# Kernel optimization log

Measured on AMD Instinct MI355X. Metric: run time of the kernel, lower is better.

Reference implementation:

```python
import jax, jax.numpy as jnp
import numpy as np

B, N, F_IN = 32, 1024, 64   # batch, num_nodes, diffusion_size[0]
K = 3                        # expansion_step
H = 2                        # num_heads
HID, RAW, OUT, CLS = 128, 128, 128, 2
D1, D2 = 128, 128            # diffusion_size[1], diffusion_size[2]
CAT = D1 + RAW               # concat dim fed to attention (h || h_prime) = 256


def setup_inputs() -> dict:
    key = jax.random.key(0)
    ks = jax.random.split(key, 40)
    g = lambda i, shape: jax.random.normal(ks[i], shape, dtype=jnp.float32) * 0.05
    inp = {
        'X': jax.random.normal(ks[0], (B, N, F_IN), dtype=jnp.float32),
        'A': jax.random.uniform(ks[1], (B, N, N), dtype=jnp.float32),
        # transition tensors / mixing weights (only the 2 layers used in forward)
        'T': g(2, (2, K, N, N)),
        'theta': jnp.full((2, K), 1.0 / K, dtype=jnp.float32),
        # raw feature projection
        'W_raw': g(3, (F_IN, RAW)), 'b_raw': jnp.zeros((RAW,), jnp.float32),
        # diffusion layer linears
        'Wd0': g(4, (F_IN, D1)), 'bd0': jnp.zeros((D1,), jnp.float32),
        'Wd1': g(5, (D1, D2)),   'bd1': jnp.zeros((D2,), jnp.float32),
        # final classifier
        'W_fin': g(6, (OUT, CLS)), 'b_fin': jnp.zeros((CLS,), jnp.float32),
    }
    # two CatMultiAttn blocks: q/k/v projections (CAT->HID), out proj (HID->OUT)
    i = 7
    for l in range(2):
        for nm in ('q', 'k', 'v'):
            inp[f'W{nm}{l}'] = g(i, (CAT, HID)); i += 1
            inp[f'b{nm}{l}'] = jnp.zeros((HID,), jnp.float32)
        inp[f'Wo{l}'] = g(i, (HID, OUT)); i += 1
        inp[f'bo{l}'] = jnp.zeros((OUT,), jnp.float32)
    return inp


def _diffusion(theta_l, T_l, h, A, W, b):
    # Q = sum_k theta_k * T_k  (generalized graph diffusion transition)
    Q = jnp.einsum('k,kij->ij', theta_l, T_l)          # [N,N]
    S = Q[None, :, :] * A                               # [B,N,N] mask by adjacency
    z = jnp.einsum('bij,bjf->bif', S, h)                # diffuse features
    return jax.nn.relu(z @ W + b)


def _cat_attn(h, hp, Wq, bq, Wk, bk, Wv, bv, Wo, bo):
    # concatenate diffused + embedding features, multi-head self-attn over nodes
    x = jnp.concatenate([h, hp], axis=-1)               # [B,N,CAT]
    b, n, _ = x.shape
    q = (x @ Wq + bq).reshape(b, n, H, HID // H)
    k = (x @ Wk + bk).reshape(b, n, H, HID // H)
    v = (x @ Wv + bv).reshape(b, n, H, HID // H)
    scale = jnp.asarray(1.0 / np.sqrt(HID // H), x.dtype)
    s = jnp.einsum('bnhd,bmhd->bhnm', q, k) * scale     # [B,H,N,N]
    p = jax.nn.softmax(s, axis=-1)
    ctx = jnp.einsum('bhnm,bmhd->bnhd', p, v).reshape(b, n, HID)
    return jax.nn.relu(ctx @ Wo + bo)


def reference(X, A, T, theta, W_raw, b_raw, Wd0, bd0, Wd1, bd1,
              W_fin, b_fin,
              Wq0, bq0, Wk0, bk0, Wv0, bv0, Wo0, bo0,
              Wq1, bq1, Wk1, bk1, Wv1, bv1, Wo1, bo1):
    theta_soft = jax.nn.softmax(theta, axis=-1)         # [2,K]
    h_prime = X @ W_raw + b_raw                          # [B,N,RAW]
    # layer 0
    h = _diffusion(theta_soft[0], T[0], X, A, Wd0, bd0)  # [B,N,D1]
    h_prime = _cat_attn(h, h_prime, Wq0, bq0, Wk0, bk0, Wv0, bv0, Wo0, bo0)
    # layer 1 (residual fusion)
    h = _diffusion(theta_soft[1], T[1], h, A, Wd1, bd1)  # [B,N,D2]
    h_prime = h_prime + _cat_attn(h, h_prime, Wq1, bq1, Wk1, bk1, Wv1, bv1, Wo1, bo1)
    return h_prime @ W_fin + b_fin                       # [B,N,CLS]
```

## Files before the change

### kernel.cpp

```cpp
#include <hip/hip_runtime.h>
#include <hip/hip_bf16.h>

typedef __hip_bfloat16 bf16;
typedef __attribute__((ext_vector_type(8))) short s8b;
typedef __attribute__((ext_vector_type(4))) short s4b;
typedef __attribute__((ext_vector_type(4))) float f4;

#define BB   32
#define NN   1024
#define FIN  64
#define HEADS 2
#define DH   64
#define HIDD 128
#define SZQ  ((size_t)BB * NN * HIDD)

__device__ __forceinline__ ushort f2bf(float x) {
    bf16 h = __float2bfloat16(x);
    return *(ushort*)&h;
}
__device__ __forceinline__ float bfbits2f(ushort h) {
    union { uint u; float f; } c; c.u = (uint)h << 16; return c.f;
}
__device__ __forceinline__ uint pk_bf16(float lo, float hi) {
    return (uint)f2bf(lo) | ((uint)f2bf(hi) << 16);
}
union U8 { short s[8]; s8b v; };
union U4 { short s[4]; s4b v; };
union UQ { ushort u[8]; s8b v; };

__global__ __launch_bounds__(256) void setup_kernel(
        const float* __restrict__ raw, const float* __restrict__ d0,
        const float* __restrict__ d1,
        const float* __restrict__ q0w, const float* __restrict__ k0w,
        const float* __restrict__ v0w, const float* __restrict__ o0w,
        const float* __restrict__ q1w, const float* __restrict__ k1w,
        const float* __restrict__ v1w, const float* __restrict__ o1w,
        ushort* __restrict__ Whi, ushort* __restrict__ Wlo,
        const float* __restrict__ T, const float* __restrict__ theta,
        ushort* __restrict__ Q0hi, ushort* __restrict__ Q0lo,
        ushort* __restrict__ Q1hi, ushort* __restrict__ Q1lo,
        const float* __restrict__ X,
        ushort* __restrict__ XT_hi, ushort* __restrict__ XT_lo) {
    __shared__ float tile[64][65];
    const int bid = blockIdx.x;
    const int t = threadIdx.x;
    if (bid < 1024) {
        int id = bid * 256 + t;
        const float* src; int K, off;
        if      (id <   8192) { src = raw; K =  64; off = 0; }
        else if (id <  16384) { src = d0;  K =  64; off = 8192; }
        else if (id <  32768) { src = d1;  K = 128; off = 16384; }
        else if (id <  65536) { src = q0w; K = 256; off = 32768; }
        else if (id <  98304) { src = k0w; K = 256; off = 65536; }
        else if (id < 131072) { src = v0w; K = 256; off = 98304; }
        else if (id < 147456) { src = o0w; K = 128; off = 131072; }
        else if (id < 180224) { src = q1w; K = 256; off = 147456; }
        else if (id < 212992) { src = k1w; K = 256; off = 180224; }
        else if (id < 245760) { src = v1w; K = 256; off = 212992; }
        else                  { src = o1w; K = 128; off = 245760; }
        int il = id - off;
        int k = il >> 7, c = il & 127;
        float w = src[il];
        ushort h = f2bf(w);
        Whi[off + c * K + k] = h;
        Wlo[off + c * K + k] = f2bf(w - bfbits2f(h));
    } else if (bid < 1536) {
        const int tb = bid - 1024;
        const int b  = tb >> 4;
        const int n0 = (tb & 15) * 64;
        {
            int nl = t >> 2, f0 = (t & 3) * 16;
            const float* xp = X + ((size_t)b * NN + n0 + nl) * 64 + f0;
#pragma unroll
            for (int i = 0; i < 16; i += 4)
                *(float4*)&tile[nl][f0 + i] = *(const float4*)(xp + i);
        }
        __syncthreads();
        {
            int f = t >> 2, n1 = (t & 3) * 16;
            U8 h0, h1, l0, l1;
#pragma unroll
            for (int i = 0; i < 16; i++) {
                float v = tile[n1 + i][f];
                ushort hh = f2bf(v);
                ushort ll = f2bf(v - bfbits2f(hh));
                if (i < 8) { h0.s[i] = (short)hh; l0.s[i] = (short)ll; }
                else       { h1.s[i - 8] = (short)hh; l1.s[i - 8] = (short)ll; }
            }
            size_t gb = ((size_t)b * 64 + f) * NN + n0 + n1;
            *(s8b*)&XT_hi[gb]     = h0.v;  *(s8b*)&XT_hi[gb + 8] = h1.v;
            *(s8b*)&XT_lo[gb]     = l0.v;  *(s8b*)&XT_lo[gb + 8] = l1.v;
        }
    } else {
        const int layer = (bid < 2048) ? 0 : 1;
        ushort* Qhi = layer ? Q1hi : Q0hi;
        ushort* Qlo = layer ? Q1lo : Q0lo;
        float t0 = theta[layer * 3 + 0];
        float t1 = theta[layer * 3 + 1];
        float t2 = theta[layer * 3 + 2];
        float m  = fmaxf(t0, fmaxf(t1, t2));
        float e0 = expf(t0 - m), e1 = expf(t1 - m), e2 = expf(t2 - m);
        float inv = 1.0f / (e0 + e1 + e2);
        e0 *= inv; e1 *= inv; e2 *= inv;
        size_t base = ((size_t)((bid - 1536) & 511) * 256 + t) * 8;
        const float* Tl = T + (size_t)layer * 3 * NN * NN;
        U8 hi, lo;
#pragma unroll
        for (int i = 0; i < 8; i++) {
            float q = e0 * Tl[base + i]
                    + e1 * Tl[base + i + (size_t)NN * NN]
                    + e2 * Tl[base + i + (size_t)2 * NN * NN];
            ushort hh = f2bf(q);
            hi.s[i] = (short)hh;
            lo.s[i] = (short)f2bf(q - bfbits2f(hh));
        }
        *(s8b*)&Qhi[base] = hi.v;
        *(s8b*)&Qlo[base] = lo.v;
    }
}

template<int F>
__global__ __launch_bounds__(512, 4) void diffusion_mfma_kernel(
        const ushort* __restrict__ Qhi, const ushort* __restrict__ Qlo,
        const float* __restrict__ A,
        const ushort* __restrict__ hT_hi, const ushort* __restrict__ hT_lo,
        float* __restrict__ z) {
    constexpr int SS  = 72;
    constexpr int NT  = F / 16;
    constexpr int TPW = NT / 2;
    __shared__ short Shi[64][SS], Slo[64][SS];
    __shared__ short Hhi[F][SS],  Hlo[F][SS];

    const int b  = blockIdx.x >> 4;
    const int i0 = (blockIdx.x & 15) * 64;
    const int t  = threadIdx.x;
    const int w  = t >> 6, lane = t & 63;
    const int quad = lane >> 4, c = lane & 15;
    const int mt = w >> 1, nh = w & 1;

    const int srow = t >> 3, scol = (t & 7) * 8;
    const float*  Ap = A   + ((size_t)b * NN + i0 + srow) * NN + scol;
    const ushort* Qh = Qhi + (size_t)(i0 + srow) * NN + scol;
    const ushort* Ql = Qlo + (size_t)(i0 + srow) * NN + scol;
    constexpr int HTR = 512 / F;
    constexpr int HJ  = 64 / HTR;
    constexpr int HV  = HJ / 8;
    const int hrow = t / HTR, hcol = (t % HTR) * HJ;
    const ushort* Hh = hT_hi + ((size_t)b * F + hrow) * NN + hcol;
    const ushort* Hl = hT_lo + ((size_t)b * F + hrow) * NN + hcol;

    f4 acc[TPW];
#pragma unroll
    for (int i = 0; i < TPW; i++) acc[i] = (f4){0.f, 0.f, 0.f, 0.f};

    float4 a0 = *(const float4*)Ap, a1 = *(const float4*)(Ap + 4);
    s8b hhv[HV], hlv[HV];
#pragma unroll
    for (int vv = 0; vv < HV; vv++) {
        hhv[vv] = *(const s8b*)(Hh + 8 * vv);
        hlv[vv] = *(const s8b*)(Hl + 8 * vv);
    }

#pragma unroll 1
    for (int j0 = 0; j0 < NN; j0 += 64) {
        UQ qh, ql;
        qh.v = *(const s8b*)(Qh + j0);
        ql.v = *(const s8b*)(Ql + j0);
        __syncthreads();
        {
            float av[8] = {a0.x, a0.y, a0.z, a0.w, a1.x, a1.y, a1.z, a1.w};
            U8 hi, lo;
#pragma unroll
            for (int i = 0; i < 8; i++) {
                float q = bfbits2f(qh.u[i]) + bfbits2f(ql.u[i]);
                float s = q * av[i];
                ushort hb = f2bf(s);
                hi.s[i] = (short)hb;
                lo.s[i] = (short)f2bf(s - bfbits2f(hb));
            }
            *(s8b*)&Shi[srow][scol] = hi.v;
            *(s8b*)&Slo[srow][scol] = lo.v;
#pragma unroll
            for (int vv = 0; vv < HV; vv++) {
                *(s8b*)&Hhi[hrow][hcol + 8 * vv] = hhv[vv];
                *(s8b*)&Hlo[hrow][hcol + 8 * vv] = hlv[vv];
            }
        }
        if (j0 + 64 < NN) {
            a0 = *(const float4*)(Ap + j0 + 64);
            a1 = *(const float4*)(Ap + j0 + 68);
#pragma unroll
            for (int vv = 0; vv < HV; vv++) {
                hhv[vv] = *(const s8b*)(Hh + j0 + 64 + 8 * vv);
                hlv[vv] = *(const s8b*)(Hl + j0 + 64 + 8 * vv);
            }
        }
        __syncthreads();

#pragma unroll
        for (int ks = 0; ks < 2; ks++) {
            s8b ahi = *(const s8b*)&Shi[mt * 16 + c][ks * 32 + quad * 8];
            s8b alo = *(const s8b*)&Slo[mt * 16 + c][ks * 32 + quad * 8];
#pragma unroll
            for (int tt = 0; tt < TPW; tt++) {
                const int nt = nh * TPW + tt;
                s8b bhi = *(const s8b*)&Hhi[nt * 16 + c][ks * 32 + quad * 8];
                s8b blo = *(const s8b*)&Hlo[nt * 16 + c][ks * 32 + quad * 8];
                acc[tt] = __builtin_amdgcn_mfma_f32_16x16x32_bf16(ahi, bhi, acc[tt], 0, 0, 0);
                acc[tt] = __builtin_amdgcn_mfma_f32_16x16x32_bf16(alo, bhi, acc[tt], 0, 0, 0);
                acc[tt] = __builtin_amdgcn_mfma_f32_16x16x32_bf16(ahi, blo, acc[tt], 0, 0, 0);
            }
        }
    }
#pragma unroll
    for (int tt = 0; tt < TPW; tt++)
#pragma unroll
        for (int r = 0; r < 4; r++)
            z[((size_t)b * NN + i0 + mt * 16 + quad * 4 + r) * F + (nh * TPW + tt) * 16 + c] = acc[tt][r];
}

template<int K1, int K2, int CB, bool RELU, bool RESID, int OMODE>
__global__ __launch_bounds__(256) void dense_mfma_kernel(
        const float* __restrict__ in1, const float* __restrict__ in2,
        const ushort* __restrict__ WT_hi, const ushort* __restrict__ WT_lo,
        const float* __restrict__ bias, const float* __restrict__ biask,
        const float* __restrict__ biasv,
        float* __restrict__ out, ushort* __restrict__ outq,
        ushort* __restrict__ hiT, ushort* __restrict__ loT,
        const float* __restrict__ Wfin, const float* __restrict__ bfin,
        float* __restrict__ fout) {
    constexpr int KD  = K1 + K2;
    constexpr int NKT = KD / 32;
    constexpr int NCT = CB / 16;
    __shared__ short Xhi[64][40], Xlo[64][40];
    __shared__ short Whi[CB][40], Wlo[CB][40];

    const int r0 = blockIdx.x * 64;
    const int c0 = blockIdx.y * CB;
    const int t  = threadIdx.x;
    const int w  = t >> 6, lane = t & 63;
    const int quad = lane >> 4, c = lane & 15;

    f4 acc[NCT];
#pragma unroll
    for (int i = 0; i < NCT; i++) acc[i] = (f4){0.f, 0.f, 0.f, 0.f};

    for (int kt = 0; kt < NKT; kt++) {
        const int k0 = kt * 32;
        __syncthreads();
        {
            int row = t >> 2, kk = (t & 3) * 8;
            int g = r0 + row;
            const float* p;
            if (K2 > 0) {
                int k = k0 + kk;
                p = (k < K1) ? (in1 + (size_t)g * K1 + k)
                             : (in2 + (size_t)g * K2 + (k - K1));
            } else {
                p = in1 + (size_t)g * K1 + k0 + kk;
            }
            float4 a = *(const float4*)p, bq = *(const float4*)(p + 4);
            float sv[8] = {a.x, a.y, a.z, a.w, bq.x, bq.y, bq.z, bq.w};
            U8 hi, lo;
#pragma unroll
            for (int i = 0; i < 8; i++) {
                ushort hh = f2bf(sv[i]);
                hi.s[i] = (short)hh;
                lo.s[i] = (short)f2bf(sv[i] - bfbits2f(hh));
            }
            *(s8b*)&Xhi[row][kk] = hi.v;
            *(s8b*)&Xlo[row][kk] = lo.v;
        }
        {
#pragma unroll
            for (int p = 0; p < CB / 64; p++) {
                int cc = p * 64 + (t >> 2), kk = (t & 3) * 8;
                size_t gsrc = (size_t)(c0 + cc) * KD + k0 + kk;
                *(s8b*)&Whi[cc][kk] = *(const s8b*)&WT_hi[gsrc];
                *(s8b*)&Wlo[cc][kk] = *(const s8b*)&WT_lo[gsrc];
            }
        }
        __syncthreads();

        s8b ah = *(const s8b*)&Xhi[16 * w + c][quad * 8];
        s8b al = *(const s8b*)&Xlo[16 * w + c][quad * 8];
#pragma unroll
        for (int ct = 0; ct < NCT; ct++) {
            s8b bh = *(const s8b*)&Whi[ct * 16 + c][quad * 8];
            s8b bl = *(const s8b*)&Wlo[ct * 16 + c][quad * 8];
            acc[ct] = __builtin_amdgcn_mfma_f32_16x16x32_bf16(ah, bh, acc[ct], 0, 0, 0);
            acc[ct] = __builtin_amdgcn_mfma_f32_16x16x32_bf16(al, bh, acc[ct], 0, 0, 0);
            acc[ct] = __builtin_amdgcn_mfma_f32_16x16x32_bf16(ah, bl, acc[ct], 0, 0, 0);
        }
    }

    const int row_g0 = r0 + 16 * w + quad * 4;
    if (OMODE == 3) {
        float fc0[4] = {0.f, 0.f, 0.f, 0.f};
        float fc1[4] = {0.f, 0.f, 0.f, 0.f};
#pragma unroll
        for (int ct = 0; ct < NCT; ct++) {
            const int col = c0 + ct * 16 + c;
            float bv = bias[col];
            float w0 = Wfin[col * 2], w1 = Wfin[col * 2 + 1];
#pragma unroll
            for (int r = 0; r < 4; r++) {
                float v = acc[ct][r] + bv;
                if (RELU) v = fmaxf(v, 0.f);
                if (RESID) v += out[(size_t)(row_g0 + r) * 128 + col];
                fc0[r] += v * w0;
                fc1[r] += v * w1;
            }
        }
#pragma unroll
        for (int r = 0; r < 4; r++) {
            float a0 = fc0[r], a1 = fc1[r];
#pragma unroll
            for (int off = 1; off < 16; off <<= 1) {
                a0 += __shfl_xor(a0, off, 16);
                a1 += __shfl_xor(a1, off, 16);
            }
            if (c == 0) {
                size_t row = row_g0 + r;
                fout[row * 2]     = a0 + bfin[0];
                fout[row * 2 + 1] = a1 + bfin[1];
            }
        }
        return;
    }
#pragma unroll
    for (int ct = 0; ct < NCT; ct++) {
        const int col = c0 + ct * 16 + c;
        if (OMODE == 1) {
            int tensor = col >> 7, cc2 = col & 127;
            float bv = (tensor == 0 ? bias : tensor == 1 ? biask : biasv)[cc2];
            int head = cc2 >> 6, d = cc2 & 63;
            int b = row_g0 >> 10, n = row_g0 & 1023;
            if (tensor == 2) {
                U4 pk;
#pragma unroll
                for (int r = 0; r < 4; r++) pk.s[r] = (short)f2bf(acc[ct][r] + bv);
                size_t addr = (((size_t)b * HEADS + head) * 64 + d) * NN + n;
                *(s4b*)&outq[2 * SZQ + addr] = pk.v;
            } else {
                ushort* dst = outq + (size_t)tensor * SZQ
                            + (((size_t)b * HEADS + head) * NN + n) * 64 + d;
#pragma unroll
                for (int r = 0; r < 4; r++) dst[(size_t)r * 64] = f2bf(acc[ct][r] + bv);
            }
        } else {
            float bv = bias[col];
            float vv[4];
#pragma unroll
            for (int r = 0; r < 4; r++) {
                float v = acc[ct][r] + bv;
                if (RELU) v = fmaxf(v, 0.f);
                size_t o = (size_t)(row_g0 + r) * 128 + col;
                if (RESID) v += out[o];
                out[o] = v;
                vv[r] = v;
            }
            if (OMODE == 2) {
                int b = row_g0 >> 10, n = row_g0 & 1023;
                U4 ph, pl;
#pragma unroll
                for (int r = 0; r < 4; r++) {
                    ushort hh = f2bf(vv[r]);
                    ph.s[r] = (short)hh;
                    pl.s[r] = (short)f2bf(vv[r] - bfbits2f(hh));
                }
                size_t tb = ((size_t)b * 128 + col) * NN + n;
                *(s4b*)&hiT[tb] = ph.v;
                *(s4b*)&loT[tb] = pl.v;
            }
        }
    }
}

__global__ __launch_bounds__(256) void attn_mfma_kernel(const ushort* __restrict__ q,
                                                        const ushort* __restrict__ k,
                                                        const ushort* __restrict__ vt,
                                                        float* __restrict__ ctx) {
    __shared__ short Ks[128][72];
    __shared__ short Vt[64][136];

    const int bh = blockIdx.x >> 4;
    const int n0 = (blockIdx.x & 15) * 64;
    const int b  = bh >> 1, h = bh & 1;
    const int t  = threadIdx.x;
    const int w  = t >> 6;
    const int lane = t & 63;
    const int quad = lane >> 4, c = lane & 15;
    const size_t kvbase = (size_t)bh * NN * 64;
    const float scale = 0.125f;

    s8b qf0, qf1;
    {
        const ushort* qrow = q + kvbase + (size_t)(n0 + 16 * w + c) * 64;
        qf0 = *(const s8b*)(qrow + quad * 8);
        qf1 = *(const s8b*)(qrow + 32 + quad * 8);
    }

    f4 O[4];
#pragma unroll
    for (int i = 0; i < 4; i++) O[i] = (f4){0.f, 0.f, 0.f, 0.f};
    float l_i = 0.f;

    for (int kt0 = 0; kt0 < NN; kt0 += 128) {
        __syncthreads();
        {
            int key = t >> 2, d0 = (t & 3) * 16;
#pragma unroll
            for (int half = 0; half < 2; half++) {
                const ushort* kr = k + kvbase + (size_t)(kt0 + 64 * half + key) * 64 + d0;
                *(s8b*)&Ks[64 * half + key][d0]     = *(const s8b*)kr;
                *(s8b*)&Ks[64 * half + key][d0 + 8] = *(const s8b*)(kr + 8);
            }
            int d = t >> 2, ch = (t & 3) * 32;
            const ushort* vr = vt + kvbase + (size_t)d * NN + kt0 + ch;
            *(s8b*)&Vt[d][ch]      = *(const s8b*)vr;
            *(s8b*)&Vt[d][ch + 8]  = *(const s8b*)(vr + 8);
            *(s8b*)&Vt[d][ch + 16] = *(const s8b*)(vr + 16);
            *(s8b*)&Vt[d][ch + 24] = *(const s8b*)(vr + 24);
        }
        __syncthreads();

        f4 sg[4][2];
#pragma unroll
        for (int g = 0; g < 4; g++) {
            const int kb = g * 32;
            sg[g][0] = (f4){0.f, 0.f, 0.f, 0.f};
            sg[g][1] = (f4){0.f, 0.f, 0.f, 0.f};
#pragma unroll
            for (int ch = 0; ch < 2; ch++) {
                s8b ka = *(const s8b*)&Ks[kb + c][ch * 32 + quad * 8];
                s8b kB = *(const s8b*)&Ks[kb + 16 + c][ch * 32 + quad * 8];
                s8b qf = ch ? qf1 : qf0;
                sg[g][0] = __builtin_amdgcn_mfma_f32_16x16x32_bf16(ka, qf, sg[g][0], 0, 0, 0);
                sg[g][1] = __builtin_amdgcn_mfma_f32_16x16x32_bf16(kB, qf, sg[g][1], 0, 0, 0);
            }
        }
        float pv[4][8];
        float ps = 0.f;
#pragma unroll
        for (int g = 0; g < 4; g++)
#pragma unroll
            for (int r = 0; r < 4; r++) {
                pv[g][r]     = __expf(sg[g][0][r] * scale);
                pv[g][4 + r] = __expf(sg[g][1][r] * scale);
                ps += pv[g][r] + pv[g][4 + r];
            }
        ps += __shfl_xor(ps, 16);
        ps += __shfl_xor(ps, 32);
        l_i += ps;

        int addr0 = ((((2 * quad) & 3) << 4) | c) << 2;
        int addr1 = ((((2 * quad + 1) & 3) << 4) | c) << 2;
        int tsel = quad >> 1;
#pragma unroll
        for (int g = 0; g < 4; g++) {
            const int kb = g * 32;
            uint Da01 = pk_bf16(pv[g][0], pv[g][1]), Da23 = pk_bf16(pv[g][2], pv[g][3]);
            uint Db01 = pk_bf16(pv[g][4], pv[g][5]), Db23 = pk_bf16(pv[g][6], pv[g][7]);
            int A01_0 = __builtin_amdgcn_ds_bpermute(addr0, (int)Da01);
            int A23_0 = __builtin_amdgcn_ds_bpermute(addr0, (int)Da23);
            int B01_0 = __builtin_amdgcn_ds_bpermute(addr0, (int)Db01);
            int B23_0 = __builtin_amdgcn_ds_bpermute(addr0, (int)Db23);
            int A01_1 = __builtin_amdgcn_ds_bpermute(addr1, (int)Da01);
            int A23_1 = __builtin_amdgcn_ds_bpermute(addr1, (int)Da23);
            int B01_1 = __builtin_amdgcn_ds_bpermute(addr1, (int)Db01);
            int B23_1 = __builtin_amdgcn_ds_bpermute(addr1, (int)Db23);
            union { int i[4]; s8b s; } pf;
            pf.i[0] = tsel ? B01_0 : A01_0;
            pf.i[1] = tsel ? B23_0 : A23_0;
            pf.i[2] = tsel ? B01_1 : A01_1;
            pf.i[3] = tsel ? B23_1 : A23_1;
#pragma unroll
            for (int dt = 0; dt < 4; dt++) {
                s8b vf = *(const s8b*)&Vt[16 * dt + c][kb + quad * 8];
                O[dt] = __builtin_amdgcn_mfma_f32_16x16x32_bf16(vf, pf.s, O[dt], 0, 0, 0);
            }
        }
    }

    float inv = 1.0f / l_i;
    float* crow = ctx + ((size_t)b * NN + n0 + 16 * w + c) * HIDD + h * DH;
#pragma unroll
    for (int dt = 0; dt < 4; dt++)
#pragma unroll
        for (int r = 0; r < 4; r++)
            crow[16 * dt + 4 * quad + r] = O[dt][r] * inv;
}

extern "C" void kernel_launch(void* const* d_in, const int* in_sizes, int n_in,
                              void* d_out, int out_size, void* d_ws, size_t ws_size,
                              hipStream_t stream) {
    (void)in_sizes; (void)n_in; (void)out_size; (void)ws_size;
    const float* X     = (const float*)d_in[0];
    const float* A     = (const float*)d_in[1];
    const float* T     = (const float*)d_in[2];
    const float* theta = (const float*)d_in[3];
    const float* W_raw = (const float*)d_in[4];
    const float* b_raw = (const float*)d_in[5];
    const float* Wd0   = (const float*)d_in[6];
    const float* bd0   = (const float*)d_in[7];
    const float* Wd1   = (const float*)d_in[8];
    const float* bd1   = (const float*)d_in[9];
    const float* W_fin = (const float*)d_in[10];
    const float* b_fin = (const float*)d_in[11];
    const float* Wq0 = (const float*)d_in[12]; const float* bq0 = (const float*)d_in[13];
    const float* Wk0 = (const float*)d_in[14]; const float* bk0 = (const float*)d_in[15];
    const float* Wv0 = (const float*)d_in[16]; const float* bv0 = (const float*)d_in[17];
    const float* Wo0 = (const float*)d_in[18]; const float* bo0 = (const float*)d_in[19];
    const float* Wq1 = (const float*)d_in[20]; const float* bq1 = (const float*)d_in[21];
    const float* Wk1 = (const float*)d_in[22]; const float* bk1 = (const float*)d_in[23];
    const float* Wv1 = (const float*)d_in[24]; const float* bv1 = (const float*)d_in[25];
    const float* Wo1 = (const float*)d_in[26]; const float* bo1 = (const float*)d_in[27];

    float* ws   = (float*)d_ws;
    const size_t SZ = (size_t)BB * NN * HIDD;
    ushort* Q0hi = (ushort*)ws;
    ushort* Q0lo = Q0hi + (size_t)NN * NN;
    float* hp   = ws + (size_t)NN * NN;
    float* h    = hp + SZ;
    float* z    = h + SZ;
    ushort* qb  = (ushort*)(z + SZ);
    ushort* kb  = qb + SZ;
    ushort* XT_hi = qb + 3 * SZ;
    ushort* XT_lo = XT_hi + SZ / 2;
    ushort* hT_hi = XT_lo + SZ / 2;
    ushort* hT_lo = hT_hi + SZ;
    ushort* WT_hi = hT_lo + SZ;
    ushort* WT_lo = WT_hi + 262144;
    ushort* Q1hi = WT_lo + 262144;
    ushort* Q1lo = Q1hi + (size_t)NN * NN;

    const int OFF_RAW = 0, OFF_D0 = 8192, OFF_D1 = 16384, OFF_QKV0 = 32768,
              OFF_O0 = 131072, OFF_QKV1 = 147456, OFF_O1 = 245760;

    const int attnGrid = BB * HEADS * (NN / 64);
    const int diffGrid = BB * (NN / 64);
    const dim3 dg1(512, 1), dg2(512, 2);

    setup_kernel<<<2560, 256, 0, stream>>>(W_raw, Wd0, Wd1, Wq0, Wk0, Wv0, Wo0,
                                           Wq1, Wk1, Wv1, Wo1, WT_hi, WT_lo,
                                           T, theta, Q0hi, Q0lo, Q1hi, Q1lo,
                                           X, XT_hi, XT_lo);

    dense_mfma_kernel<64, 0, 128, false, false, 0><<<dg1, 256, 0, stream>>>(
        X, nullptr, WT_hi + OFF_RAW, WT_lo + OFF_RAW, b_raw, nullptr, nullptr,
        hp, nullptr, nullptr, nullptr, nullptr, nullptr, nullptr);
    diffusion_mfma_kernel<64><<<diffGrid, 512, 0, stream>>>(Q0hi, Q0lo, A, XT_hi, XT_lo, z);
    dense_mfma_kernel<64, 0, 128, true, false, 2><<<dg1, 256, 0, stream>>>(
        z, nullptr, WT_hi + OFF_D0, WT_lo + OFF_D0, bd0, nullptr, nullptr,
        h, nullptr, hT_hi, hT_lo, nullptr, nullptr, nullptr);
    dense_mfma_kernel<128, 128, 192, false, false, 1><<<dg2, 256, 0, stream>>>(
        h, hp, WT_hi + OFF_QKV0, WT_lo + OFF_QKV0, bq0, bk0, bv0,
        nullptr, qb, nullptr, nullptr, nullptr, nullptr, nullptr);
    attn_mfma_kernel<<<attnGrid, 256, 0, stream>>>(qb, kb, qb + 2 * SZ, z);
    dense_mfma_kernel<128, 0, 128, true, false, 0><<<dg1, 256, 0, stream>>>(
        z, nullptr, WT_hi + OFF_O0, WT_lo + OFF_O0, bo0, nullptr, nullptr,
        hp, nullptr, nullptr, nullptr, nullptr, nullptr, nullptr);

    diffusion_mfma_kernel<128><<<diffGrid, 512, 0, stream>>>(Q1hi, Q1lo, A, hT_hi, hT_lo, z);
    dense_mfma_kernel<128, 0, 128, true, false, 0><<<dg1, 256, 0, stream>>>(
        z, nullptr, WT_hi + OFF_D1, WT_lo + OFF_D1, bd1, nullptr, nullptr,
        h, nullptr, nullptr, nullptr, nullptr, nullptr, nullptr);
    dense_mfma_kernel<128, 128, 192, false, false, 1><<<dg2, 256, 0, stream>>>(
        h, hp, WT_hi + OFF_QKV1, WT_lo + OFF_QKV1, bq1, bk1, bv1,
        nullptr, qb, nullptr, nullptr, nullptr, nullptr, nullptr);
    attn_mfma_kernel<<<attnGrid, 256, 0, stream>>>(qb, kb, qb + 2 * SZ, z);
    dense_mfma_kernel<128, 0, 128, true, true, 3><<<dg1, 256, 0, stream>>>(
        z, nullptr, WT_hi + OFF_O1, WT_lo + OFF_O1, bo1, nullptr, nullptr,
        hp, nullptr, nullptr, nullptr, W_fin, b_fin, (float*)d_out);
}
```

Measured before the change: 526.5 us.

## Use 2x-row warp tiles in MFMA kernels and remap block order

The diffusion and dense MFMA kernels now give each wave a 32-row by N-column register tile (two 16-row subtiles) instead of one 16-row strip. Each B fragment loaded from LDS is reused across two A fragments, which cuts LDS read traffic per MFMA. The dense kernel's final-classifier epilogue now needs a shared-memory reduction across column halves plus an extra barrier. The diffusion and attention kernels also remap blockIdx so consecutive blocks go to different batches, likely to spread work across XCDs and L2. The larger accumulator tiles raise register pressure and may lower occupancy.

```diff
diff --git a/kernel.cpp b/kernel.cpp
--- a/kernel.cpp
+++ b/kernel.cpp
@@ -127,16 +127,19 @@
         float* __restrict__ z) {
     constexpr int SS  = 72;
     constexpr int NT  = F / 16;
-    constexpr int TPW = NT / 2;
+    constexpr int NCW = NT / 4;
     __shared__ short Shi[64][SS], Slo[64][SS];
     __shared__ short Hhi[F][SS],  Hlo[F][SS];
 
-    const int b  = blockIdx.x >> 4;
-    const int i0 = (blockIdx.x & 15) * 64;
+    const int bidx = blockIdx.x;
+    const int u  = bidx >> 3;
+    const int b  = (bidx & 7) + 8 * (u >> 4);
+    const int i0 = (u & 15) * 64;
     const int t  = threadIdx.x;
     const int w  = t >> 6, lane = t & 63;
     const int quad = lane >> 4, c = lane & 15;
-    const int mt = w >> 1, nh = w & 1;
+    const int rh = w >> 2;
+    const int ch = w & 3;
 
     const int srow = t >> 3, scol = (t & 7) * 8;
     const float*  Ap = A   + ((size_t)b * NN + i0 + srow) * NN + scol;
@@ -149,9 +152,11 @@
     const ushort* Hh = hT_hi + ((size_t)b * F + hrow) * NN + hcol;
     const ushort* Hl = hT_lo + ((size_t)b * F + hrow) * NN + hcol;
 
-    f4 acc[TPW];
-#pragma unroll
-    for (int i = 0; i < TPW; i++) acc[i] = (f4){0.f, 0.f, 0.f, 0.f};
+    f4 acc[2][NCW];
+#pragma unroll
+    for (int st = 0; st < 2; st++)
+#pragma unroll
+        for (int i = 0; i < NCW; i++) acc[st][i] = (f4){0.f, 0.f, 0.f, 0.f};
 
     float4 a0 = *(const float4*)Ap, a1 = *(const float4*)(Ap + 4);
     s8b hhv[HV], hlv[HV];
@@ -199,24 +204,32 @@
 
 #pragma unroll
         for (int ks = 0; ks < 2; ks++) {
-            s8b ahi = *(const s8b*)&Shi[mt * 16 + c][ks * 32 + quad * 8];
-            s8b alo = *(const s8b*)&Slo[mt * 16 + c][ks * 32 + quad * 8];
-#pragma unroll
-            for (int tt = 0; tt < TPW; tt++) {
-                const int nt = nh * TPW + tt;
+            s8b ah0 = *(const s8b*)&Shi[32 * rh + c][ks * 32 + quad * 8];
+            s8b al0 = *(const s8b*)&Slo[32 * rh + c][ks * 32 + quad * 8];
+            s8b ah1 = *(const s8b*)&Shi[32 * rh + 16 + c][ks * 32 + quad * 8];
+            s8b al1 = *(const s8b*)&Slo[32 * rh + 16 + c][ks * 32 + quad * 8];
+#pragma unroll
+            for (int ctn = 0; ctn < NCW; ctn++) {
+                const int nt = ch * NCW + ctn;
                 s8b bhi = *(const s8b*)&Hhi[nt * 16 + c][ks * 32 + quad * 8];
                 s8b blo = *(const s8b*)&Hlo[nt * 16 + c][ks * 32 + quad * 8];
-                acc[tt] = __builtin_amdgcn_mfma_f32_16x16x32_bf16(ahi, bhi, acc[tt], 0, 0, 0);
-                acc[tt] = __builtin_amdgcn_mfma_f32_16x16x32_bf16(alo, bhi, acc[tt], 0, 0, 0);
-                acc[tt] = __builtin_amdgcn_mfma_f32_16x16x32_bf16(ahi, blo, acc[tt], 0, 0, 0);
-            }
-        }
-    }
-#pragma unroll
-    for (int tt = 0; tt < TPW; tt++)
-#pragma unroll
-        for (int r = 0; r < 4; r++)
-            z[((size_t)b * NN + i0 + mt * 16 + quad * 4 + r) * F + (nh * TPW + tt) * 16 + c] = acc[tt][r];
+                acc[0][ctn] = __builtin_amdgcn_mfma_f32_16x16x32_bf16(ah0, bhi, acc[0][ctn], 0, 0, 0);
+                acc[0][ctn] = __builtin_amdgcn_mfma_f32_16x16x32_bf16(al0, bhi, acc[0][ctn], 0, 0, 0);
+                acc[0][ctn] = __builtin_amdgcn_mfma_f32_16x16x32_bf16(ah0, blo, acc[0][ctn], 0, 0, 0);
+                acc[1][ctn] = __builtin_amdgcn_mfma_f32_16x16x32_bf16(ah1, bhi, acc[1][ctn], 0, 0, 0);
+                acc[1][ctn] = __builtin_amdgcn_mfma_f32_16x16x32_bf16(al1, bhi, acc[1][ctn], 0, 0, 0);
+                acc[1][ctn] = __builtin_amdgcn_mfma_f32_16x16x32_bf16(ah1, blo, acc[1][ctn], 0, 0, 0);
+            }
+        }
+    }
+#pragma unroll
+    for (int st = 0; st < 2; st++)
+#pragma unroll
+        for (int ctn = 0; ctn < NCW; ctn++)
+#pragma unroll
+            for (int r = 0; r < 4; r++)
+                z[((size_t)b * NN + i0 + 32 * rh + 16 * st + quad * 4 + r) * F
+                  + (ch * NCW + ctn) * 16 + c] = acc[st][ctn][r];
 }
 
 template<int K1, int K2, int CB, bool RELU, bool RESID, int OMODE>
@@ -231,19 +244,24 @@
         float* __restrict__ fout) {
     constexpr int KD  = K1 + K2;
     constexpr int NKT = KD / 32;
-    constexpr int NCT = CB / 16;
+    constexpr int NCH = CB / 32;
     __shared__ short Xhi[64][40], Xlo[64][40];
     __shared__ short Whi[CB][40], Wlo[CB][40];
+    __shared__ float red[64][2];
 
     const int r0 = blockIdx.x * 64;
     const int c0 = blockIdx.y * CB;
     const int t  = threadIdx.x;
     const int w  = t >> 6, lane = t & 63;
     const int quad = lane >> 4, c = lane & 15;
-
-    f4 acc[NCT];
-#pragma unroll
-    for (int i = 0; i < NCT; i++) acc[i] = (f4){0.f, 0.f, 0.f, 0.f};
+    const int rh = w >> 1;
+    const int ch = w & 1;
+
+    f4 acc[2][NCH];
+#pragma unroll
+    for (int st = 0; st < 2; st++)
+#pragma unroll
+        for (int i = 0; i < NCH; i++) acc[st][i] = (f4){0.f, 0.f, 0.f, 0.f};
 
     for (int kt = 0; kt < NKT; kt++) {
         const int k0 = kt * 32;
@@ -282,96 +300,133 @@
         }
         __syncthreads();
 
-        s8b ah = *(const s8b*)&Xhi[16 * w + c][quad * 8];
-        s8b al = *(const s8b*)&Xlo[16 * w + c][quad * 8];
-#pragma unroll
-        for (int ct = 0; ct < NCT; ct++) {
-            s8b bh = *(const s8b*)&Whi[ct * 16 + c][quad * 8];
-            s8b bl = *(const s8b*)&Wlo[ct * 16 + c][quad * 8];
-            acc[ct] = __builtin_amdgcn_mfma_f32_16x16x32_bf16(ah, bh, acc[ct], 0, 0, 0);
-            acc[ct] = __builtin_amdgcn_mfma_f32_16x16x32_bf16(al, bh, acc[ct], 0, 0, 0);
-            acc[ct] = __builtin_amdgcn_mfma_f32_16x16x32_bf16(ah, bl, acc[ct], 0, 0, 0);
-        }
-    }
-
-    const int row_g0 = r0 + 16 * w + quad * 4;
+        s8b ah0 = *(const s8b*)&Xhi[32 * rh + c][quad * 8];
+        s8b al0 = *(const s8b*)&Xlo[32 * rh + c][quad * 8];
+        s8b ah1 = *(const s8b*)&Xhi[32 * rh + 16 + c][quad * 8];
+        s8b al1 = *(const s8b*)&Xlo[32 * rh + 16 + c][quad * 8];
+#pragma unroll
+        for (int ct = 0; ct < NCH; ct++) {
+            s8b bh = *(const s8b*)&Whi[ch * (CB / 2) + ct * 16 + c][quad * 8];
+            s8b bl = *(const s8b*)&Wlo[ch * (CB / 2) + ct * 16 + c][quad * 8];
+            acc[0][ct] = __builtin_amdgcn_mfma_f32_16x16x32_bf16(ah0, bh, acc[0][ct], 0, 0, 0);
+            acc[0][ct] = __builtin_amdgcn_mfma_f32_16x16x32_bf16(al0, bh, acc[0][ct], 0, 0, 0);
+            acc[0][ct] = __builtin_amdgcn_mfma_f32_16x16x32_bf16(ah0, bl, acc[0][ct], 0, 0, 0);
+            acc[1][ct] = __builtin_amdgcn_mfma_f32_16x16x32_bf16(ah1, bh, acc[1][ct], 0, 0, 0);
+            acc[1][ct] = __builtin_amdgcn_mfma_f32_16x16x32_bf16(al1, bh, acc[1][ct], 0, 0, 0);
+            acc[1][ct] = __builtin_amdgcn_mfma_f32_16x16x32_bf16(ah1, bl, acc[1][ct], 0, 0, 0);
+        }
+    }
+
     if (OMODE == 3) {
-        float fc0[4] = {0.f, 0.f, 0.f, 0.f};
-        float fc1[4] = {0.f, 0.f, 0.f, 0.f};
-#pragma unroll
-        for (int ct = 0; ct < NCT; ct++) {
-            const int col = c0 + ct * 16 + c;
+        float fc[2][2][4];
+#pragma unroll
+        for (int st = 0; st < 2; st++)
+#pragma unroll
+            for (int o = 0; o < 2; o++)
+#pragma unroll
+                for (int r = 0; r < 4; r++) fc[st][o][r] = 0.f;
+#pragma unroll
+        for (int ct = 0; ct < NCH; ct++) {
+            const int col = c0 + ch * (CB / 2) + ct * 16 + c;
             float bv = bias[col];
             float w0 = Wfin[col * 2], w1 = Wfin[col * 2 + 1];
 #pragma unroll
+            for (int st = 0; st < 2; st++) {
+                const int rg = r0 + 32 * rh + 16 * st + quad * 4;
+#pragma unroll
+                for (int r = 0; r < 4; r++) {
+                    float v = acc[st][ct][r] + bv;
+                    if (RELU) v = fmaxf(v, 0.f);
+                    if (RESID) v += out[(size_t)(rg + r) * 128 + col];
+                    fc[st][0][r] += v * w0;
+                    fc[st][1][r] += v * w1;
+                }
+            }
+        }
+#pragma unroll
+        for (int st = 0; st < 2; st++)
+#pragma unroll
             for (int r = 0; r < 4; r++) {
-                float v = acc[ct][r] + bv;
-                if (RELU) v = fmaxf(v, 0.f);
-                if (RESID) v += out[(size_t)(row_g0 + r) * 128 + col];
-                fc0[r] += v * w0;
-                fc1[r] += v * w1;
-            }
-        }
-#pragma unroll
-        for (int r = 0; r < 4; r++) {
-            float a0 = fc0[r], a1 = fc1[r];
-#pragma unroll
-            for (int off = 1; off < 16; off <<= 1) {
-                a0 += __shfl_xor(a0, off, 16);
-                a1 += __shfl_xor(a1, off, 16);
-            }
-            if (c == 0) {
-                size_t row = row_g0 + r;
-                fout[row * 2]     = a0 + bfin[0];
-                fout[row * 2 + 1] = a1 + bfin[1];
-            }
+                float a0 = fc[st][0][r], a1 = fc[st][1][r];
+#pragma unroll
+                for (int off = 1; off < 16; off <<= 1) {
+                    a0 += __shfl_xor(a0, off, 16);
+                    a1 += __shfl_xor(a1, off, 16);
+                }
+                fc[st][0][r] = a0; fc[st][1][r] = a1;
+            }
+        if (ch == 1 && c == 0) {
+#pragma unroll
+            for (int st = 0; st < 2; st++)
+#pragma unroll
+                for (int r = 0; r < 4; r++) {
+                    int lr = 32 * rh + 16 * st + quad * 4 + r;
+                    red[lr][0] = fc[st][0][r];
+                    red[lr][1] = fc[st][1][r];
+                }
+        }
+        __syncthreads();
+        if (ch == 0 && c == 0) {
+#pragma unroll
+            for (int st = 0; st < 2; st++)
+#pragma unroll
+                for (int r = 0; r < 4; r++) {
+                    int lr = 32 * rh + 16 * st + quad * 4 + r;
+                    size_t row = (size_t)r0 + lr;
+                    fout[row * 2]     = fc[st][0][r] + red[lr][0] + bfin[0];
+                    fout[row * 2 + 1] = fc[st][1][r] + red[lr][1] + bfin[1];
+                }
         }
         return;
     }
 #pragma unroll
-    for (int ct = 0; ct < NCT; ct++) {
-        const int col = c0 + ct * 16 + c;
-        if (OMODE == 1) {
-            int tensor = col >> 7, cc2 = col & 127;
-            float bv = (tensor == 0 ? bias : tensor == 1 ? biask : biasv)[cc2];
-            int head = cc2 >> 6, d = cc2 & 63;
-            int b = row_g0 >> 10, n = row_g0 & 1023;
-            if (tensor == 2) {
-                U4 pk;
-#pragma unroll
-                for (int r = 0; r < 4; r++) pk.s[r] = (short)f2bf(acc[ct][r] + bv);
-                size_t addr = (((size_t)b * HEADS + head) * 64 + d) * NN + n;
-                *(s4b*)&outq[2 * SZQ + addr] = pk.v;
+    for (int st = 0; st < 2; st++) {
+        const int row_g0 = r0 + 32 * rh + 16 * st + quad * 4;
+#pragma unroll
+        for (int ct = 0; ct < NCH; ct++) {
+            const int col = c0 + ch * (CB / 2) + ct * 16 + c;
+            if (OMODE == 1) {
+                int tensor = col >> 7, cc2 = col & 127;
+                float bv = (tensor == 0 ? bias : tensor == 1 ? biask : biasv)[cc2];
+                int head = cc2 >> 6, d = cc2 & 63;
+                int b = row_g0 >> 10, n = row_g0 & 1023;
+                if (tensor == 2) {
+                    U4 pk;
+#pragma unroll
+                    for (int r = 0; r < 4; r++) pk.s[r] = (short)f2bf(acc[st][ct][r] + bv);
+                    size_t addr = (((size_t)b * HEADS + head) * 64 + d) * NN + n;
+                    *(s4b*)&outq[2 * SZQ + addr] = pk.v;
+                } else {
+                    ushort* dst = outq + (size_t)tensor * SZQ
+                                + (((size_t)b * HEADS + head) * NN + n) * 64 + d;
+#pragma unroll
+                    for (int r = 0; r < 4; r++) dst[(size_t)r * 64] = f2bf(acc[st][ct][r] + bv);
+                }
             } else {
-                ushort* dst = outq + (size_t)tensor * SZQ
-                            + (((size_t)b * HEADS + head) * NN + n) * 64 + d;
-#pragma unroll
-                for (int r = 0; r < 4; r++) dst[(size_t)r * 64] = f2bf(acc[ct][r] + bv);
-            }
-        } else {
-            float bv = bias[col];
-            float vv[4];
-#pragma unroll
-            for (int r = 0; r < 4; r++) {
-                float v = acc[ct][r] + bv;
-                if (RELU) v = fmaxf(v, 0.f);
-                size_t o = (size_t)(row_g0 + r) * 128 + col;
-                if (RESID) v += out[o];
-                out[o] = v;
-                vv[r] = v;
-            }
-            if (OMODE == 2) {
-                int b = row_g0 >> 10, n = row_g0 & 1023;
-                U4 ph, pl;
+                float bv = bias[col];
+                float vv[4];
 #pragma unroll
                 for (int r = 0; r < 4; r++) {
-                    ushort hh = f2bf(vv[r]);
-                    ph.s[r] = (short)hh;
-                    pl.s[r] = (short)f2bf(vv[r] - bfbits2f(hh));
+                    float v = acc[st][ct][r] + bv;
+                    if (RELU) v = fmaxf(v, 0.f);
+                    size_t o = (size_t)(row_g0 + r) * 128 + col;
+                    if (RESID) v += out[o];
+                    out[o] = v;
+                    vv[r] = v;
                 }
-                size_t tb = ((size_t)b * 128 + col) * NN + n;
-                *(s4b*)&hiT[tb] = ph.v;
-                *(s4b*)&loT[tb] = pl.v;
+                if (OMODE == 2) {
+                    int b = row_g0 >> 10, n = row_g0 & 1023;
+                    U4 ph, pl;
+#pragma unroll
+                    for (int r = 0; r < 4; r++) {
+                        ushort hh = f2bf(vv[r]);
+                        ph.s[r] = (short)hh;
+                        pl.s[r] = (short)f2bf(vv[r] - bfbits2f(hh));
+                    }
+                    size_t tb = ((size_t)b * 128 + col) * NN + n;
+                    *(s4b*)&hiT[tb] = ph.v;
+                    *(s4b*)&loT[tb] = pl.v;
+                }
             }
         }
     }
@@ -384,8 +439,10 @@
     __shared__ short Ks[128][72];
     __shared__ short Vt[64][136];
 
-    const int bh = blockIdx.x >> 4;
-    const int n0 = (blockIdx.x & 15) * 64;
+    const int bidx = blockIdx.x;
+    const int u  = bidx >> 3;
+    const int bh = (bidx & 7) + 8 * (u >> 4);
+    const int n0 = (u & 15) * 64;
     const int b  = bh >> 1, h = bh & 1;
     const int t  = threadIdx.x;
     const int w  = t >> 6;
```

Result: faster. 512.6 us (-2.6%).
